# Optimization experiments

Measured on AMD Instinct MI355X. Metric: run time of the kernel, lower is better.

The kernel has to match this reference:

```python
import jax, jax.numpy as jnp
import numpy as np

B, T, N, NF, H, C, E = 4, 16, 4096, 8, 64, 13, 131072
NUM_HEADS = 4


def setup_inputs() -> dict:
    key = jax.random.key(0)
    ks = jax.random.split(key, 32)
    s = 0.05

    def w(k, shape):
        return (jax.random.normal(k, shape, jnp.float32) * s)

    p = {}
    p["node_features"] = jax.random.normal(ks[0], (B, T, N, NF), jnp.float32)
    p["edge_index_seq"] = jax.random.randint(ks[1], (T, 2, E), 0, N)
    # spatial_conv: Linear(NF,H) -> ReLU -> Linear(H,H)
    p["sc_w1"] = w(ks[2], (H, NF)); p["sc_b1"] = w(ks[3], (H,))
    p["sc_w2"] = w(ks[4], (H, H)); p["sc_b2"] = w(ks[5], (H,))
    # 2-layer LSTM (eval mode, dropout inactive); gate order i,f,g,o
    p["w_ih0"] = w(ks[6], (4 * H, H)); p["w_hh0"] = w(ks[7], (4 * H, H))
    p["b_ih0"] = w(ks[8], (4 * H,)); p["b_hh0"] = w(ks[9], (4 * H,))
    p["w_ih1"] = w(ks[10], (4 * H, H)); p["w_hh1"] = w(ks[11], (4 * H, H))
    p["b_ih1"] = w(ks[12], (4 * H,)); p["b_hh1"] = w(ks[13], (4 * H,))
    # MultiheadAttention (packed in-proj like torch)
    p["attn_in_w"] = w(ks[14], (3 * H, H)); p["attn_in_b"] = w(ks[15], (3 * H,))
    p["attn_out_w"] = w(ks[16], (H, H)); p["attn_out_b"] = w(ks[17], (H,))
    # predictor MLP (dropout inactive in eval)
    p["pw1"] = w(ks[18], (2 * H, H)); p["pb1"] = w(ks[19], (2 * H,))
    p["pw2"] = w(ks[20], (H, 2 * H)); p["pb2"] = w(ks[21], (H,))
    p["pw3"] = w(ks[22], (C, H)); p["pb3"] = w(ks[23], (C,))
    return p


def _message_pass(h_t, edges, n_nodes):
    # h_t: [B, N, H]; edges: [2, E]
    src, dst = edges[0], edges[1]
    msgs = h_t[:, src, :]  # gather pre-update embeddings, [B, E, H]
    sums = jax.vmap(lambda m: jax.ops.segment_sum(m, dst, num_segments=n_nodes))(msgs)
    cnt = jax.ops.segment_sum(jnp.ones(dst.shape, h_t.dtype), dst, num_segments=n_nodes)
    mean = sums / jnp.maximum(cnt, 1.0)[None, :, None]
    has_msg = (cnt > 0)[None, :, None]
    return jnp.where(has_msg, (h_t + mean) * 0.5, h_t)


def _lstm_layer(x, wi, wh, bi, bh):
    # x: [M, T, H] -> [M, T, H]
    M = x.shape[0]
    Hh = wh.shape[1]
    xg = x @ wi.T + bi  # precompute input contribution, [M, T, 4H]
    def step(carry, xg_t):
        hp, cp = carry
        g = xg_t + hp @ wh.T + bh
        i, f, gg, o = jnp.split(g, 4, axis=-1)
        i = jax.nn.sigmoid(i); f = jax.nn.sigmoid(f)
        gg = jnp.tanh(gg); o = jax.nn.sigmoid(o)
        c = f * cp + i * gg
        hn = o * jnp.tanh(c)
        return (hn, c), hn
    init = (jnp.zeros((M, Hh), x.dtype), jnp.zeros((M, Hh), x.dtype))
    _, hs = jax.lax.scan(step, init, xg.transpose(1, 0, 2))
    return hs.transpose(1, 0, 2)


def reference(node_features, edge_index_seq, sc_w1, sc_b1, sc_w2, sc_b2,
              w_ih0, w_hh0, b_ih0, b_hh0, w_ih1, w_hh1, b_ih1, b_hh1,
              attn_in_w, attn_in_b, attn_out_w, attn_out_b,
              pw1, pb1, pw2, pb2, pw3, pb3):
    Bs, Ts, Ns, _ = node_features.shape
    Hh = sc_w1.shape[0]

    # spatial conv over all timesteps at once: [B, T, N, H]
    h = jax.nn.relu(node_features @ sc_w1.T + sc_b1) @ sc_w2.T + sc_b2

    # per-timestep gather + segment-mean message passing (memory-bound core)
    def step(_, inp):
        h_t, e_t = inp
        return None, _message_pass(h_t, e_t, Ns)
    _, h_mp = jax.lax.scan(step, None, (h.transpose(1, 0, 2, 3), edge_index_seq))
    spatial_stack = h_mp.transpose(1, 0, 2, 3)  # [B, T, N, H]

    # LSTM over time per (batch, node)
    x = spatial_stack.transpose(0, 2, 1, 3).reshape(Bs * Ns, Ts, Hh)
    x = _lstm_layer(x, w_ih0, w_hh0, b_ih0, b_hh0)
    x = _lstm_layer(x, w_ih1, w_hh1, b_ih1, b_hh1)

    # self-attention (torch MHA, batch_first)
    qkv = x @ attn_in_w.T + attn_in_b
    q, k, v = jnp.split(qkv, 3, axis=-1)
    hd = Hh // NUM_HEADS
    def heads(z):
        return z.reshape(Bs * Ns, Ts, NUM_HEADS, hd).transpose(0, 2, 1, 3)
    q, k, v = heads(q), heads(k), heads(v)
    scores = jnp.einsum('mhqd,mhkd->mhqk', q, k) / np.float32(np.sqrt(hd))
    attn = jax.nn.softmax(scores, axis=-1)
    o = jnp.einsum('mhqk,mhkd->mhqd', attn, v)
    o = o.transpose(0, 2, 1, 3).reshape(Bs * Ns, Ts, Hh)
    o = o @ attn_out_w.T + attn_out_b

    final_hidden = o[:, -1, :]
    z = jax.nn.relu(final_hidden @ pw1.T + pb1)
    z = jax.nn.relu(z @ pw2.T + pb2)
    logits = z @ pw3.T + pb3
    return logits.reshape(Bs, Ns, -1)
```

## Files before the change

### kernel.cpp

```cpp
#include <hip/hip_runtime.h>

#define Bq 4
#define Tq 16
#define Nq 4096
#define NFq 8
#define Hq 64
#define Eq 131072
#define Cq 13
#define Mq (Bq*Nq)

typedef __attribute__((ext_vector_type(8))) short bf16x8;
typedef __attribute__((ext_vector_type(4))) float f32x4;

__device__ __forceinline__ float bf2f(unsigned short u) {
  return __uint_as_float(((unsigned int)u) << 16);
}
__device__ __forceinline__ unsigned short f2bf(float f) {
  unsigned int x = __float_as_uint(f);
  unsigned int r = x + 0x7fff + ((x >> 16) & 1);
  return (unsigned short)(r >> 16);
}
__device__ __forceinline__ float rcpf(float x) {
  float r;
  asm("v_rcp_f32 %0, %1" : "=v"(r) : "v"(x));
  return r;
}
__device__ __forceinline__ float sigf(float x) {
  return rcpf(1.f + __expf(-x));
}
__device__ __forceinline__ float tanh_c(float x) {
  float e = __expf(-2.f * x);
  return 2.f * rcpf(1.f + e) - 1.f;
}
__device__ __forceinline__ unsigned int pk_bf16(float lo, float hi) {
  unsigned int r;
  asm("v_cvt_pk_bf16_f32 %0, %1, %2" : "=v"(r) : "v"(lo), "v"(hi));
  return r;
}
__device__ __forceinline__ float dot2bf(unsigned int a, unsigned int b, float c) {
  float r;
  asm("v_dot2_f32_bf16 %0, %1, %2, %3" : "=v"(r) : "v"(a), "v"(b), "v"(c));
  return r;
}

#define O_BC0  65536
#define O_BC1  65792
#define O_QB   70144
#define O_VB   74304
#define O_B1P  95872

#define WB_AQT  0
#define WB_AWK  4096
#define WB_WVT  8192
#define WB_P1OW 12288
#define WB_P2T  20480
#define WB_P3T  28672
#define WB_TOT  29696

#define AQT_P   0
#define WVT_P   2048
#define P1OW_P  4096
#define P2T_P   8192
#define WAVE_SCR 3648
#define SMEM_ATTN (49152 + 8 * WAVE_SCR)

__global__ __launch_bounds__(256) void k_prep(
    const float* __restrict__ bih0, const float* __restrict__ bhh0,
    const float* __restrict__ bih1, const float* __restrict__ bhh1,
    float* __restrict__ wT) {
  int i = threadIdx.x;
  wT[O_BC0 + i] = bih0[i] + bhh0[i];
  wT[O_BC1 + i] = bih1[i] + bhh1[i];
}

__global__ __launch_bounds__(256) void k_prep_wa(
    const float* __restrict__ wih0, const float* __restrict__ whh0,
    const float* __restrict__ wih1, const float* __restrict__ whh1,
    unsigned short* __restrict__ WA) {
  int i = blockIdx.x * 256 + threadIdx.x;
  int j = i & 7, lane = (i >> 3) & 63, ks = (i >> 9) & 3;
  int mt = (i >> 11) & 15, L = (i >> 15) & 1;
  int rp = 16 * mt + (lane & 15);
  int orig = (rp & 3) * 64 + (rp >> 2);
  int k = 32 * ks + 8 * (lane >> 4) + j;
  const float* w = L ? (k < 64 ? wih1 : whh1) : (k < 64 ? wih0 : whh0);
  WA[i] = f2bf(w[orig * 64 + (k & 63)]);
}

__global__ __launch_bounds__(256) void k_prep2(
    const float* __restrict__ aw, const float* __restrict__ ab,
    const float* __restrict__ pw2, const float* __restrict__ pw3,
    unsigned short* __restrict__ WBu, float* __restrict__ wT) {
  int i = blockIdx.x * 256 + threadIdx.x;
  if (i < 4096) {
    int k = i >> 6, ch = i & 63;
    int pidx = (k >> 1) * 128 + ch * 2 + (k & 1);
    WBu[WB_AQT + pidx] = f2bf(0.25f * aw[ch * 64 + k]);
    WBu[WB_AWK + i]    = f2bf(aw[(64 + k) * 64 + ch]);
    WBu[WB_WVT + pidx] = f2bf(aw[(128 + ch) * 64 + k]);
  }
  {
    int k = i >> 6, j = i & 63;
    int pidx = (k >> 1) * 128 + j * 2 + (k & 1);
    WBu[WB_P2T + pidx] = f2bf(pw2[j * 128 + k]);
  }
  if (i < 1024) {
    int k = i >> 4, c = i & 15;
    int pidx = (k >> 1) * 32 + c * 2 + (k & 1);
    WBu[WB_P3T + pidx] = (c < 13) ? f2bf(pw3[c * 64 + k]) : (unsigned short)0;
  }
  if (i < 64) {
    wT[O_QB + i] = 0.25f * ab[i];
    wT[O_VB + i] = ab[128 + i];
  }
}

__global__ __launch_bounds__(256) void k_prep3(
    const float* __restrict__ pw1, const float* __restrict__ ow,
    const float* __restrict__ ob, const float* __restrict__ pb1,
    unsigned short* __restrict__ WBu, float* __restrict__ wT) {
  int i = blockIdx.x * 256 + threadIdx.x;
  int j = i >> 6, k = i & 63;
  float s0 = 0.f, s1 = 0.f, s2 = 0.f, s3 = 0.f;
  for (int m2 = 0; m2 < 64; m2 += 4) {
    s0 += pw1[j * 64 + m2]     * ow[m2 * 64 + k];
    s1 += pw1[j * 64 + m2 + 1] * ow[(m2 + 1) * 64 + k];
    s2 += pw1[j * 64 + m2 + 2] * ow[(m2 + 2) * 64 + k];
    s3 += pw1[j * 64 + m2 + 3] * ow[(m2 + 3) * 64 + k];
  }
  WBu[WB_P1OW + (k >> 1) * 256 + j * 2 + (k & 1)] = f2bf((s0 + s1) + (s2 + s3));
  if (k == 0) {
    float b = pb1[j];
    for (int m2 = 0; m2 < 64; ++m2) b += pw1[j * 64 + m2] * ob[m2];
    wT[O_B1P + j] = b;
  }
}

__global__ __launch_bounds__(256) void k_enc(
    const float* __restrict__ nf, const float* __restrict__ w1,
    const float* __restrict__ b1, const float* __restrict__ w2,
    const float* __restrict__ b2, unsigned short* __restrict__ henc) {
  __shared__ float xr[64][9];
  __shared__ float w1l[64][8];
  __shared__ float b1l[64];
  __shared__ float w2l[4096];
  __shared__ float b2l[64];
  __shared__ float h1l[64 * 65];
  __shared__ unsigned short OUT[64 * 68];
  int tid = threadIdx.x;
  size_t row0 = (size_t)blockIdx.x * 64;
  if (tid < 128) {
    float4 v = ((const float4*)w1)[tid];
    int j = tid >> 1, q = tid & 1;
    w1l[j][q * 4] = v.x; w1l[j][q * 4 + 1] = v.y;
    w1l[j][q * 4 + 2] = v.z; w1l[j][q * 4 + 3] = v.w;
  }
  if (tid < 64) { b1l[tid] = b1[tid]; b2l[tid] = b2[tid]; }
  {
    const float4* s = (const float4*)w2;
    #pragma unroll
    for (int u = 0; u < 4; ++u) {
      float4 v = s[tid + u * 256];
      int base = (tid + u * 256) * 4;
      w2l[base] = v.x; w2l[base + 1] = v.y; w2l[base + 2] = v.z; w2l[base + 3] = v.w;
    }
  }
  if (tid < 128) {
    float4 v = ((const float4*)(nf + row0 * 8))[tid];
    int r = tid >> 1, q = tid & 1;
    xr[r][q * 4] = v.x; xr[r][q * 4 + 1] = v.y;
    xr[r][q * 4 + 2] = v.z; xr[r][q * 4 + 3] = v.w;
  }
  __syncthreads();
  int r = tid & 63, co = tid >> 6;
  #pragma unroll
  for (int jj = 0; jj < 16; ++jj) {
    int j = co * 16 + jj;
    float acc = b1l[j];
    #pragma unroll
    for (int k = 0; k < 8; ++k) acc += w1l[j][k] * xr[r][k];
    h1l[r * 65 + j] = fmaxf(acc, 0.f);
  }
  __syncthreads();
  float acc[16];
  #pragma unroll
  for (int jj = 0; jj < 16; ++jj) acc[jj] = b2l[co * 16 + jj];
  for (int k = 0; k < 64; ++k) {
    float xv = h1l[r * 65 + k];
    #pragma unroll
    for (int jj = 0; jj < 16; ++jj)
      acc[jj] += w2l[(co * 16 + jj) * 64 + k] * xv;
  }
  #pragma unroll
  for (int jj = 0; jj < 16; jj += 2) {
    unsigned int pk = (unsigned int)f2bf(acc[jj]) | ((unsigned int)f2bf(acc[jj + 1]) << 16);
    *(unsigned int*)(&OUT[r * 68 + co * 16 + jj]) = pk;
  }
  __syncthreads();
  {
    int rr = tid >> 2, part = tid & 3;
    uint2 a = *(uint2*)(&OUT[rr * 68 + part * 16]);
    uint2 b = *(uint2*)(&OUT[rr * 68 + part * 16 + 4]);
    uint4 v; v.x = a.x; v.y = a.y; v.z = b.x; v.w = b.y;
    *(uint4*)(henc + (row0 + rr) * 64 + part * 16) = v;
  }
}

__global__ __launch_bounds__(1024) void k_count(const int* __restrict__ ei,
                                                int* __restrict__ bhist) {
  __shared__ int hist[4096];
  int b = blockIdx.x;
  int t = b & 15, seg = b >> 4;
  int tid = threadIdx.x;
  #pragma unroll
  for (int i = tid; i < 4096; i += 1024) hist[i] = 0;
  __syncthreads();
  const int* dstp = ei + ((t << 1) + 1) * Eq + (seg << 13);
  #pragma unroll
  for (int u = 0; u < 8; ++u) {
    int dst = dstp[(u << 10) + tid];
    atomicAdd(&hist[dst], 1);
  }
  __syncthreads();
  int* op = bhist + (b << 12);
  #pragma unroll
  for (int i = tid; i < 4096; i += 1024) op[i] = hist[i];
}

__global__ __launch_bounds__(256) void k_scan(const int* __restrict__ bhist,
                                              int* __restrict__ rp,
                                              int* __restrict__ segoff) {
  int t = blockIdx.x, tid = threadIdx.x;
  __shared__ int part[256];
  int loc[16];
  int s = 0;
  #pragma unroll
  for (int j = 0; j < 16; ++j) {
    int node = tid * 16 + j;
    int v = 0;
    #pragma unroll
    for (int seg = 0; seg < 16; ++seg)
      v += bhist[((t + (seg << 4)) << 12) + node];
    loc[j] = v;
    s += v;
  }
  part[tid] = s;
  __syncthreads();
  if (tid == 0) {
    int run = 0;
    for (int i2 = 0; i2 < 256; ++i2) { int v = part[i2]; part[i2] = run; run += v; }
  }
  __syncthreads();
  int off = part[tid];
  #pragma unroll
  for (int j = 0; j < 16; ++j) {
    int node = tid * 16 + j;
    rp[t * (Nq + 1) + node] = off;
    int running = off;
    #pragma unroll
    for (int seg = 0; seg < 16; ++seg) {
      segoff[(((t << 4) + seg) << 12) + node] = running;
      running += bhist[((t + (seg << 4)) << 12) + node];
    }
    off += loc[j];
  }
  if (tid == 255) rp[t * (Nq + 1) + Nq] = off;
}

__global__ __launch_bounds__(1024) void k_scatter(const int* __restrict__ ei,
    const int* __restrict__ segoff, int* __restrict__ col) {
  __shared__ int loff[4096];
  int b = blockIdx.x;
  int t = b & 15, seg = b >> 4;
  int tid = threadIdx.x;
  for (int i = tid; i < 4096; i += 1024)
    loff[i] = segoff[(((t << 4) + seg) << 12) + i];
  __syncthreads();
  const int* srcp = ei + (t << 1) * Eq + (seg << 13);
  const int* dstp = ei + ((t << 1) + 1) * Eq + (seg << 13);
  #pragma unroll
  for (int u = 0; u < 8; ++u) {
    int e = (u << 10) + tid;
    int src = srcp[e];
    int dst = dstp[e];
    int pos = atomicAdd(&loff[dst], 1);
    col[(t << 17) + pos] = src;
  }
}

__global__ __launch_bounds__(256) void k_mp(const unsigned short* __restrict__ henc,
    const int* __restrict__ rp, const int* __restrict__ col,
    unsigned short* __restrict__ hmp) {
  int lane = threadIdx.x & 63;
  int bkk = blockIdx.x;
  int t = bkk & 15;
  int n = (bkk >> 4) * 4 + __builtin_amdgcn_readfirstlane(threadIdx.x >> 6);
  const int* rpt = rp + t * (Nq + 1);
  const int* colt = col + (t << 17);
  int e0 = rpt[n], e1 = rpt[n + 1];
  int half = lane >> 5;
  int b2 = (lane >> 3) & 3;
  int c8 = (lane & 7) << 3;
  const unsigned short* hb2 = henc + (size_t)b2 * 4194304 + t * 262144 + c8;
  float acc[8] = {0.f, 0.f, 0.f, 0.f, 0.f, 0.f, 0.f, 0.f};
  int e = e0;
  for (; e + 8 <= e1; e += 8) {
    int i0 = colt[e + half];
    int i1 = colt[e + 2 + half];
    int i2 = colt[e + 4 + half];
    int i3 = colt[e + 6 + half];
    uint4 p0 = *(const uint4*)(hb2 + i0 * 64);
    uint4 p1 = *(const uint4*)(hb2 + i1 * 64);
    uint4 p2 = *(const uint4*)(hb2 + i2 * 64);
    uint4 p3 = *(const uint4*)(hb2 + i3 * 64);
    acc[0] += bf2f((unsigned short)(p0.x & 0xffff)) + bf2f((unsigned short)(p1.x & 0xffff))
            + bf2f((unsigned short)(p2.x & 0xffff)) + bf2f((unsigned short)(p3.x & 0xffff));
    acc[1] += bf2f((unsigned short)(p0.x >> 16)) + bf2f((unsigned short)(p1.x >> 16))
            + bf2f((unsigned short)(p2.x >> 16)) + bf2f((unsigned short)(p3.x >> 16));
    acc[2] += bf2f((unsigned short)(p0.y & 0xffff)) + bf2f((unsigned short)(p1.y & 0xffff))
            + bf2f((unsigned short)(p2.y & 0xffff)) + bf2f((unsigned short)(p3.y & 0xffff));
    acc[3] += bf2f((unsigned short)(p0.y >> 16)) + bf2f((unsigned short)(p1.y >> 16))
            + bf2f((unsigned short)(p2.y >> 16)) + bf2f((unsigned short)(p3.y >> 16));
    acc[4] += bf2f((unsigned short)(p0.z & 0xffff)) + bf2f((unsigned short)(p1.z & 0xffff))
            + bf2f((unsigned short)(p2.z & 0xffff)) + bf2f((unsigned short)(p3.z & 0xffff));
    acc[5] += bf2f((unsigned short)(p0.z >> 16)) + bf2f((unsigned short)(p1.z >> 16))
            + bf2f((unsigned short)(p2.z >> 16)) + bf2f((unsigned short)(p3.z >> 16));
    acc[6] += bf2f((unsigned short)(p0.w & 0xffff)) + bf2f((unsigned short)(p1.w & 0xffff))
            + bf2f((unsigned short)(p2.w & 0xffff)) + bf2f((unsigned short)(p3.w & 0xffff));
    acc[7] += bf2f((unsigned short)(p0.w >> 16)) + bf2f((unsigned short)(p1.w >> 16))
            + bf2f((unsigned short)(p2.w >> 16)) + bf2f((unsigned short)(p3.w >> 16));
  }
  if (half == 0) {
    for (; e < e1; ++e) {
      int i0 = colt[e];
      uint4 p0 = *(const uint4*)(hb2 + i0 * 64);
      acc[0] += bf2f((unsigned short)(p0.x & 0xffff));
      acc[1] += bf2f((unsigned short)(p0.x >> 16));
      acc[2] += bf2f((unsigned short)(p0.y & 0xffff));
      acc[3] += bf2f((unsigned short)(p0.y >> 16));
      acc[4] += bf2f((unsigned short)(p0.z & 0xffff));
      acc[5] += bf2f((unsigned short)(p0.z >> 16));
      acc[6] += bf2f((unsigned short)(p0.w & 0xffff));
      acc[7] += bf2f((unsigned short)(p0.w >> 16));
    }
  }
  #pragma unroll
  for (int i = 0; i < 8; ++i) acc[i] += __shfl_xor(acc[i], 32);
  uint4 ps = *(const uint4*)(hb2 + n * 64);
  int deg = e1 - e0;
  if (half == 0) {
    uint4 out;
    if (deg > 0) {
      float sc = 0.5f * rcpf((float)deg);
      float s0 = bf2f((unsigned short)(ps.x & 0xffff)) * 0.5f + acc[0] * sc;
      float s1 = bf2f((unsigned short)(ps.x >> 16))    * 0.5f + acc[1] * sc;
      float s2 = bf2f((unsigned short)(ps.y & 0xffff)) * 0.5f + acc[2] * sc;
      float s3 = bf2f((unsigned short)(ps.y >> 16))    * 0.5f + acc[3] * sc;
      float s4 = bf2f((unsigned short)(ps.z & 0xffff)) * 0.5f + acc[4] * sc;
      float s5 = bf2f((unsigned short)(ps.z >> 16))    * 0.5f + acc[5] * sc;
      float s6 = bf2f((unsigned short)(ps.w & 0xffff)) * 0.5f + acc[6] * sc;
      float s7 = bf2f((unsigned short)(ps.w >> 16))    * 0.5f + acc[7] * sc;
      out.x = pk_bf16(s0, s1);
      out.y = pk_bf16(s2, s3);
      out.z = pk_bf16(s4, s5);
      out.w = pk_bf16(s6, s7);
    } else {
      out = ps;
    }
    *(uint4*)(hmp + (size_t)b2 * 4194304 + t * 262144 + n * 64 + c8) = out;
  }
}

__global__ __launch_bounds__(1024) void k_lstm(
    const unsigned short* __restrict__ hmp,
    const unsigned short* __restrict__ WA,
    const float* __restrict__ wT,
    unsigned short* __restrict__ x2) {
  __shared__ unsigned short XF[4096];
  __shared__ unsigned short H0F[2][4096];
  __shared__ unsigned short H1F[2][4096];
  __shared__ unsigned short OUTB[64 * 68];
  int tid = threadIdx.x;
  int l = tid & 63;
  int w = tid >> 6;
  int mtp = w >> 1, ntp = w & 1;
  int m0 = blockIdx.x << 6;

  bf16x8 afr[2][2][4];
  const bf16x8* wa8 = (const bf16x8*)WA;
  #pragma unroll
  for (int L = 0; L < 2; ++L)
    #pragma unroll
    for (int mt2 = 0; mt2 < 2; ++mt2)
      #pragma unroll
      for (int ks = 0; ks < 4; ++ks)
        afr[L][mt2][ks] = wa8[((L * 16 + (2 * mtp + mt2)) * 4 + ks) * 64 + l];

  float4 bias0[2], bias1[2];
  int hbase[2], obase[2];
  #pragma unroll
  for (int mt2 = 0; mt2 < 2; ++mt2) {
    int ch = 4 * (2 * mtp + mt2) + (l >> 4);
    bias0[mt2].x = wT[O_BC0 + ch];       bias0[mt2].y = wT[O_BC0 + 64 + ch];
    bias0[mt2].z = wT[O_BC0 + 128 + ch]; bias0[mt2].w = wT[O_BC0 + 192 + ch];
    bias1[mt2].x = wT[O_BC1 + ch];       bias1[mt2].y = wT[O_BC1 + 64 + ch];
    bias1[mt2].z = wT[O_BC1 + 128 + ch]; bias1[mt2].w = wT[O_BC1 + 192 + ch];
    int l2 = (l & 15) | (((ch >> 3) & 3) << 4);
    hbase[mt2] = (ch >> 5) * 2048 + l2 * 8 + (ch & 7);
    obase[mt2] = (l & 15) * 68 + ch;
  }
  float c0a[2][2] = {{0.f, 0.f}, {0.f, 0.f}};
  float c1a[2][2] = {{0.f, 0.f}, {0.f, 0.f}};

  int sA = tid >> 4, c4 = (tid & 15) << 2;
  int xfidx = (((c4 >> 5) * 4 + (sA >> 4)) * 64 + ((sA & 15) | (((c4 >> 3) & 3) << 4))) * 8 + (c4 & 7);
  int mm = m0 + sA;
  int bb = mm >> 12, nn = mm & 4095;
  const unsigned short* srcb = hmp + ((size_t)(bb * 16) * 4096 + (size_t)nn) * 64 + c4;
  unsigned short* x2g = x2 + (size_t)mm * (Tq * Hq) + c4;
  int outsrc = sA * 68 + c4;

  int* hz0 = (int*)&H0F[0][0];
  int* hz1 = (int*)&H1F[0][0];
  for (int i = tid; i < 4096; i += 1024) { hz0[i] = 0; hz1[i] = 0; }

  uint2 xv = *(const uint2*)srcb;
  __syncthreads();

  for (int t = 0; t < Tq; ++t) {
    int cur = t & 1, prv = cur ^ 1;
    *(uint2*)(XF + xfidx) = xv;
    __syncthreads();
    if (t < Tq - 1) xv = *(const uint2*)(srcb + (t + 1) * 262144);

    {
      f32x4 acc[2][2];
      #pragma unroll
      for (int mt2 = 0; mt2 < 2; ++mt2)
        #pragma unroll
        for (int nt2 = 0; nt2 < 2; ++nt2) {
          float4 bv = bias0[mt2];
          acc[mt2][nt2] = (f32x4){bv.x, bv.y, bv.z, bv.w};
        }
      #pragma unroll
      for (int nt2 = 0; nt2 < 2; ++nt2) {
        int nt = 2 * ntp + nt2;
        #pragma unroll
        for (int ks = 0; ks < 4; ++ks) {
          const unsigned short* bs = (ks < 2) ? XF : H0F[prv];
          bf16x8 bf = *(const bf16x8*)(bs + (((ks & 1) * 4 + nt) * 64 + l) * 8);
          acc[0][nt2] = __builtin_amdgcn_mfma_f32_16x16x32_bf16(afr[0][0][ks], bf, acc[0][nt2], 0, 0, 0);
          acc[1][nt2] = __builtin_amdgcn_mfma_f32_16x16x32_bf16(afr[0][1][ks], bf, acc[1][nt2], 0, 0, 0);
        }
      }
      #pragma unroll
      for (int mt2 = 0; mt2 < 2; ++mt2) {
        float hh[2];
        #pragma unroll
        for (int nt2 = 0; nt2 < 2; ++nt2) {
          f32x4 g = acc[mt2][nt2];
          float ig = sigf(g[0]);
          float fg = sigf(g[1]);
          float gg = tanh_c(g[2]);
          float og = sigf(g[3]);
          float c = fg * c0a[mt2][nt2] + ig * gg;
          c0a[mt2][nt2] = c;
          hh[nt2] = og * tanh_c(c);
        }
        unsigned int pk = pk_bf16(hh[0], hh[1]);
        int base = hbase[mt2] + 2 * ntp * 512;
        H0F[cur][base]       = (unsigned short)pk;
        H0F[cur][base + 512] = (unsigned short)(pk >> 16);
      }
    }
    __syncthreads();

    {
      f32x4 acc[2][2];
      #pragma unroll
      for (int mt2 = 0; mt2 < 2; ++mt2)
        #pragma unroll
        for (int nt2 = 0; nt2 < 2; ++nt2) {
          float4 bv = bias1[mt2];
          acc[mt2][nt2] = (f32x4){bv.x, bv.y, bv.z, bv.w};
        }
      #pragma unroll
      for (int nt2 = 0; nt2 < 2; ++nt2) {
        int nt = 2 * ntp + nt2;
        #pragma unroll
        for (int ks = 0; ks < 4; ++ks) {
          const unsigned short* bs = (ks < 2) ? H0F[cur] : H1F[prv];
          bf16x8 bf = *(const bf16x8*)(bs + (((ks & 1) * 4 + nt) * 64 + l) * 8);
          acc[0][nt2] = __builtin_amdgcn_mfma_f32_16x16x32_bf16(afr[1][0][ks], bf, acc[0][nt2], 0, 0, 0);
          acc[1][nt2] = __builtin_amdgcn_mfma_f32_16x16x32_bf16(afr[1][1][ks], bf, acc[1][nt2], 0, 0, 0);
        }
      }
      #pragma unroll
      for (int mt2 = 0; mt2 < 2; ++mt2) {
        float hh[2];
        #pragma unroll
        for (int nt2 = 0; nt2 < 2; ++nt2) {
          f32x4 g = acc[mt2][nt2];
          float ig = sigf(g[0]);
          float fg = sigf(g[1]);
          float gg = tanh_c(g[2]);
          float og = sigf(g[3]);
          float c = fg * c1a[mt2][nt2] + ig * gg;
          c1a[mt2][nt2] = c;
          hh[nt2] = og * tanh_c(c);
        }
        unsigned int pk = pk_bf16(hh[0], hh[1]);
        int base = hbase[mt2] + 2 * ntp * 512;
        H1F[cur][base]       = (unsigned short)pk;
        H1F[cur][base + 512] = (unsigned short)(pk >> 16);
        int ob = obase[mt2] + 2 * ntp * 1088;
        OUTB[ob]        = (unsigned short)pk;
        OUTB[ob + 1088] = (unsigned short)(pk >> 16);
      }
    }
    __syncthreads();

    {
      uint2 ov = *(const uint2*)(OUTB + outsrc);
      *(uint2*)(x2g + t * 64) = ov;
    }
  }
}

__global__ __launch_bounds__(512, 4) void k_attn(const unsigned short* __restrict__ x2,
    const unsigned short* __restrict__ WB, const float* __restrict__ wp,
    const float* __restrict__ pb2, const float* __restrict__ pb3,
    float* __restrict__ outp) {
  extern __shared__ char smem[];
  unsigned int* WLu = (unsigned int*)smem;
  int tid = threadIdx.x;
  int lane = tid & 63;
  int wid = tid >> 6;
  {
    const uint4* src = (const uint4*)WB;
    uint4* dstw = (uint4*)smem;
    for (int i = tid; i < 3072; i += 512)
      dstw[i] = src[(i < 512) ? i : i + 512];
  }
  char* wbase = smem + 49152 + wid * WAVE_SCR;
  unsigned short* xw = (unsigned short*)wbase;
  float* q = (float*)(wbase + 2304);
  unsigned int* op = (unsigned int*)(wbase + 2304);
  unsigned int* qkp = (unsigned int*)(wbase + 2560);
  unsigned int* hbp = qkp;
  float* pz = (float*)(wbase + 3104);
  unsigned int* z2p = (unsigned int*)(wbase + 3104);
  unsigned int* z1p = (unsigned int*)(wbase + 3360);
  int m = (blockIdx.x << 3) + wid;
  {
    const uint4* xp = (const uint4*)(x2 + (size_t)m * 1024);
    #pragma unroll
    for (int u = 0; u < 2; ++u) {
      uint4 pv = xp[lane * 2 + u];
      int f0 = (lane * 2 + u) * 8;
      int t = f0 >> 6, ch0 = f0 & 63;
      *(uint4*)(xw + t * 72 + ch0) = pv;
    }
  }
  __syncthreads();
  {
    const unsigned short* xr = xw + 15 * 72;
    float a0 = wp[O_QB + lane], a1 = 0.f, a2 = 0.f, a3 = 0.f;
    #pragma unroll
    for (int k2 = 0; k2 < 32; k2 += 4) {
      a0 = dot2bf(WLu[AQT_P + (k2 + 0) * 64 + lane], *(const unsigned int*)(xr + 2 * (k2 + 0)), a0);
      a1 = dot2bf(WLu[AQT_P + (k2 + 1) * 64 + lane], *(const unsigned int*)(xr + 2 * (k2 + 1)), a1);
      a2 = dot2bf(WLu[AQT_P + (k2 + 2) * 64 + lane], *(const unsigned int*)(xr + 2 * (k2 + 2)), a2);
      a3 = dot2bf(WLu[AQT_P + (k2 + 3) * 64 + lane], *(const unsigned int*)(xr + 2 * (k2 + 3)), a3);
    }
    q[lane] = (a0 + a1) + (a2 + a3);
  }
  #pragma unroll
  for (int h = 0; h < 4; ++h) {
    float a0 = 0.f, a1 = 0.f, a2 = 0.f, a3 = 0.f;
    #pragma unroll
    for (int d = 0; d < 16; d += 4) {
      a0 += bf2f(WB[WB_AWK + (h * 16 + d + 0) * 64 + lane]) * q[h * 16 + d + 0];
      a1 += bf2f(WB[WB_AWK + (h * 16 + d + 1) * 64 + lane]) * q[h * 16 + d + 1];
      a2 += bf2f(WB[WB_AWK + (h * 16 + d + 2) * 64 + lane]) * q[h * 16 + d + 2];
      a3 += bf2f(WB[WB_AWK + (h * 16 + d + 3) * 64 + lane]) * q[h * 16 + d + 3];
    }
    float a = (a0 + a1) + (a2 + a3);
    float an = __shfl_xor(a, 1);
    if (!(lane & 1)) qkp[h * 33 + (lane >> 1)] = pk_bf16(a, an);
  }
  {
    int hh = lane >> 4, tt = lane & 15;
    const unsigned short* xr = xw + tt * 72;
    float a0 = 0.f, a1 = 0.f, a2 = 0.f, a3 = 0.f;
    #pragma unroll
    for (int c2 = 0; c2 < 32; c2 += 4) {
      a0 = dot2bf(qkp[hh * 33 + c2 + 0], *(const unsigned int*)(xr + 2 * (c2 + 0)), a0);
      a1 = dot2bf(qkp[hh * 33 + c2 + 1], *(const unsigned int*)(xr + 2 * (c2 + 1)), a1);
      a2 = dot2bf(qkp[hh * 33 + c2 + 2], *(const unsigned int*)(xr + 2 * (c2 + 2)), a2);
      a3 = dot2bf(qkp[hh * 33 + c2 + 3], *(const unsigned int*)(xr + 2 * (c2 + 3)), a3);
    }
    float sc = (a0 + a1) + (a2 + a3);
    float mx = sc;
    mx = fmaxf(mx, __shfl_xor(mx, 1));
    mx = fmaxf(mx, __shfl_xor(mx, 2));
    mx = fmaxf(mx, __shfl_xor(mx, 4));
    mx = fmaxf(mx, __shfl_xor(mx, 8));
    float e = __expf(sc - mx);
    float sum = e;
    sum += __shfl_xor(sum, 1);
    sum += __shfl_xor(sum, 2);
    sum += __shfl_xor(sum, 4);
    sum += __shfl_xor(sum, 8);
    pz[lane] = e * rcpf(sum);
  }
  {
    float hb0 = 0.f, hb1 = 0.f, hb2 = 0.f, hb3 = 0.f;
    #pragma unroll
    for (int t = 0; t < 16; ++t) {
      float xv = bf2f(xw[t * 72 + lane]);
      hb0 += pz[t] * xv;
      hb1 += pz[16 + t] * xv;
      hb2 += pz[32 + t] * xv;
      hb3 += pz[48 + t] * xv;
    }
    float n0 = __shfl_xor(hb0, 1);
    float n1 = __shfl_xor(hb1, 1);
    float n2 = __shfl_xor(hb2, 1);
    float n3 = __shfl_xor(hb3, 1);
    if (!(lane & 1)) {
      int p = lane >> 1;
      hbp[p]          = pk_bf16(hb0, n0);
      hbp[33 + p]     = pk_bf16(hb1, n1);
      hbp[66 + p]     = pk_bf16(hb2, n2);
      hbp[99 + p]     = pk_bf16(hb3, n3);
    }
  }
  {
    int hsel = lane >> 4;
    float a0 = wp[O_VB + lane], a1 = 0.f, a2 = 0.f, a3 = 0.f;
    #pragma unroll
    for (int k2 = 0; k2 < 32; k2 += 4) {
      a0 = dot2bf(WLu[WVT_P + (k2 + 0) * 64 + lane], hbp[hsel * 33 + k2 + 0], a0);
      a1 = dot2bf(WLu[WVT_P + (k2 + 1) * 64 + lane], hbp[hsel * 33 + k2 + 1], a1);
      a2 = dot2bf(WLu[WVT_P + (k2 + 2) * 64 + lane], hbp[hsel * 33 + k2 + 2], a2);
      a3 = dot2bf(WLu[WVT_P + (k2 + 3) * 64 + lane], hbp[hsel * 33 + k2 + 3], a3);
    }
    float o = (a0 + a1) + (a2 + a3);
    float on = __shfl_xor(o, 1);
    if (!(lane & 1)) op[lane >> 1] = pk_bf16(o, on);
  }
  {
    float a0 = wp[O_B1P + lane], a1 = 0.f;
    float b0 = wp[O_B1P + 64 + lane], b1 = 0.f;
    #pragma unroll
    for (int k2 = 0; k2 < 32; k2 += 2) {
      unsigned int ov0 = op[k2], ov1 = op[k2 + 1];
      a0 = dot2bf(WLu[P1OW_P + (k2 + 0) * 128 + lane], ov0, a0);
      a1 = dot2bf(WLu[P1OW_P + (k2 + 1) * 128 + lane], ov1, a1);
      b0 = dot2bf(WLu[P1OW_P + (k2 + 0) * 128 + 64 + lane], ov0, b0);
      b1 = dot2bf(WLu[P1OW_P + (k2 + 1) * 128 + 64 + lane], ov1, b1);
    }
    float ra = fmaxf(a0 + a1, 0.f);
    float rb = fmaxf(b0 + b1, 0.f);
    float ran = __shfl_xor(ra, 1);
    float rbn = __shfl_xor(rb, 1);
    if (!(lane & 1)) {
      z1p[lane >> 1]      = pk_bf16(ra, ran);
      z1p[32 + (lane >> 1)] = pk_bf16(rb, rbn);
    }
  }
  {
    float a0 = pb2[lane], a1 = 0.f, a2 = 0.f, a3 = 0.f;
    #pragma unroll
    for (int k2 = 0; k2 < 64; k2 += 4) {
      a0 = dot2bf(WLu[P2T_P + (k2 + 0) * 64 + lane], z1p[k2 + 0], a0);
      a1 = dot2bf(WLu[P2T_P + (k2 + 1) * 64 + lane], z1p[k2 + 1], a1);
      a2 = dot2bf(WLu[P2T_P + (k2 + 2) * 64 + lane], z1p[k2 + 2], a2);
      a3 = dot2bf(WLu[P2T_P + (k2 + 3) * 64 + lane], z1p[k2 + 3], a3);
    }
    float z2 = fmaxf((a0 + a1) + (a2 + a3), 0.f);
    float zn = __shfl_xor(z2, 1);
    if (!(lane & 1)) z2p[lane >> 1] = pk_bf16(z2, zn);
  }
  {
    const unsigned int* p3 = (const unsigned int*)(WB + WB_P3T);
    int c = lane & 15;
    float a0 = (c < 13) ? pb3[c] : 0.f, a1 = 0.f, a2 = 0.f, a3 = 0.f;
    #pragma unroll
    for (int k2 = 0; k2 < 32; k2 += 4) {
      a0 = dot2bf(p3[(k2 + 0) * 16 + c], z2p[k2 + 0], a0);
      a1 = dot2bf(p3[(k2 + 1) * 16 + c], z2p[k2 + 1], a1);
      a2 = dot2bf(p3[(k2 + 2) * 16 + c], z2p[k2 + 2], a2);
      a3 = dot2bf(p3[(k2 + 3) * 16 + c], z2p[k2 + 3], a3);
    }
    if (lane < 13) outp[(size_t)m * 13 + lane] = (a0 + a1) + (a2 + a3);
  }
}

extern "C" void kernel_launch(void* const* d_in, const int* in_sizes, int n_in,
                              void* d_out, int out_size, void* d_ws, size_t ws_size,
                              hipStream_t stream) {
  (void)in_sizes; (void)n_in; (void)out_size; (void)ws_size;
  const float* nf   = (const float*)d_in[0];
  const int*   ei   = (const int*)d_in[1];
  const float* sw1  = (const float*)d_in[2];
  const float* sb1  = (const float*)d_in[3];
  const float* sw2  = (const float*)d_in[4];
  const float* sb2  = (const float*)d_in[5];
  const float* wih0 = (const float*)d_in[6];
  const float* whh0 = (const float*)d_in[7];
  const float* bih0 = (const float*)d_in[8];
  const float* bhh0 = (const float*)d_in[9];
  const float* wih1 = (const float*)d_in[10];
  const float* whh1 = (const float*)d_in[11];
  const float* bih1 = (const float*)d_in[12];
  const float* bhh1 = (const float*)d_in[13];
  const float* aw   = (const float*)d_in[14];
  const float* ab   = (const float*)d_in[15];
  const float* ow   = (const float*)d_in[16];
  const float* ob   = (const float*)d_in[17];
  const float* pw1  = (const float*)d_in[18];
  const float* pb1  = (const float*)d_in[19];
  const float* pw2  = (const float*)d_in[20];
  const float* pb2  = (const float*)d_in[21];
  const float* pw3  = (const float*)d_in[22];
  const float* pb3  = (const float*)d_in[23];

  char* ws = (char*)d_ws;
  float* wT = (float*)ws;
  unsigned short* WA = (unsigned short*)(ws + 393216);
  unsigned short* WB = (unsigned short*)(ws + 458752);
  int* rp   = (int*)(ws + 1048576);
  int* col  = (int*)(ws + 1572864);
  unsigned short* henc = (unsigned short*)(ws + 10485760);
  unsigned short* hmp  = (unsigned short*)(ws + 44040192);
  int* bhist  = (int*)(ws + 44040192);
  int* segoff = (int*)(ws + 48234496);
  unsigned short* x2   = henc;
  float* outp = (float*)d_out;

  hipFuncSetAttribute((const void*)k_attn,
                      hipFuncAttributeMaxDynamicSharedMemorySize, SMEM_ATTN);
  k_prep<<<1, 256, 0, stream>>>(bih0, bhh0, bih1, bhh1, wT);
  k_prep_wa<<<256, 256, 0, stream>>>(wih0, whh0, wih1, whh1, WA);
  k_prep2<<<32, 256, 0, stream>>>(aw, ab, pw2, pw3, WB, wT);
  k_prep3<<<32, 256, 0, stream>>>(pw1, ow, ob, pb1, WB, wT);
  k_enc<<<4096, 256, 0, stream>>>(nf, sw1, sb1, sw2, sb2, henc);
  k_count<<<256, 1024, 0, stream>>>(ei, bhist);
  k_scan<<<16, 256, 0, stream>>>(bhist, rp, segoff);
  k_scatter<<<256, 1024, 0, stream>>>(ei, segoff, col);
  k_mp<<<16384, 256, 0, stream>>>(henc, rp, col, hmp);
  k_lstm<<<256, 1024, 0, stream>>>(hmp, WA, wT, x2);
  k_attn<<<2048, 512, SMEM_ATTN, stream>>>(x2, WB, wT, pb2, pb3, outp);
}
```

Before: 287.1 us.

## Halve LSTM block tile to 32 sequences so 512 blocks fill the GPU

The LSTM kernel now handles 32 sequences per 1024-thread block instead of 64. Each wave owns a single gate-channel m-tile across both n-tiles, and the launch grows to 512 blocks. The old 256-block grid underfills a GPU with 256 CUs and serialises the 16-step recurrence, so more blocks should give more latency hiding and better occupancy. In exchange, every block reloads the full weight fragments and shared-memory loads and stores become narrower, with more barriers per unit of work.

```diff
diff --git a/kernel.cpp b/kernel.cpp
--- a/kernel.cpp
+++ b/kernel.cpp
@@ -376,153 +376,123 @@
     const unsigned short* __restrict__ WA,
     const float* __restrict__ wT,
     unsigned short* __restrict__ x2) {
-  __shared__ unsigned short XF[4096];
-  __shared__ unsigned short H0F[2][4096];
-  __shared__ unsigned short H1F[2][4096];
-  __shared__ unsigned short OUTB[64 * 68];
+  __shared__ unsigned short XF[2048];
+  __shared__ unsigned short H0F[2][2048];
+  __shared__ unsigned short H1F[2][2048];
+  __shared__ unsigned short OUTB[32 * 68];
   int tid = threadIdx.x;
   int l = tid & 63;
-  int w = tid >> 6;
-  int mtp = w >> 1, ntp = w & 1;
-  int m0 = blockIdx.x << 6;
-
-  bf16x8 afr[2][2][4];
+  int w = __builtin_amdgcn_readfirstlane(tid >> 6);
+  int m0 = blockIdx.x << 5;
+
+  bf16x8 afr[2][4];
   const bf16x8* wa8 = (const bf16x8*)WA;
   #pragma unroll
   for (int L = 0; L < 2; ++L)
     #pragma unroll
-    for (int mt2 = 0; mt2 < 2; ++mt2)
-      #pragma unroll
-      for (int ks = 0; ks < 4; ++ks)
-        afr[L][mt2][ks] = wa8[((L * 16 + (2 * mtp + mt2)) * 4 + ks) * 64 + l];
-
-  float4 bias0[2], bias1[2];
-  int hbase[2], obase[2];
-  #pragma unroll
-  for (int mt2 = 0; mt2 < 2; ++mt2) {
-    int ch = 4 * (2 * mtp + mt2) + (l >> 4);
-    bias0[mt2].x = wT[O_BC0 + ch];       bias0[mt2].y = wT[O_BC0 + 64 + ch];
-    bias0[mt2].z = wT[O_BC0 + 128 + ch]; bias0[mt2].w = wT[O_BC0 + 192 + ch];
-    bias1[mt2].x = wT[O_BC1 + ch];       bias1[mt2].y = wT[O_BC1 + 64 + ch];
-    bias1[mt2].z = wT[O_BC1 + 128 + ch]; bias1[mt2].w = wT[O_BC1 + 192 + ch];
-    int l2 = (l & 15) | (((ch >> 3) & 3) << 4);
-    hbase[mt2] = (ch >> 5) * 2048 + l2 * 8 + (ch & 7);
-    obase[mt2] = (l & 15) * 68 + ch;
-  }
-  float c0a[2][2] = {{0.f, 0.f}, {0.f, 0.f}};
-  float c1a[2][2] = {{0.f, 0.f}, {0.f, 0.f}};
-
-  int sA = tid >> 4, c4 = (tid & 15) << 2;
-  int xfidx = (((c4 >> 5) * 4 + (sA >> 4)) * 64 + ((sA & 15) | (((c4 >> 3) & 3) << 4))) * 8 + (c4 & 7);
+    for (int ks = 0; ks < 4; ++ks)
+      afr[L][ks] = wa8[((L * 16 + w) * 4 + ks) * 64 + l];
+
+  int ch = 4 * w + (l >> 4);
+  float4 bias0, bias1;
+  bias0.x = wT[O_BC0 + ch];       bias0.y = wT[O_BC0 + 64 + ch];
+  bias0.z = wT[O_BC0 + 128 + ch]; bias0.w = wT[O_BC0 + 192 + ch];
+  bias1.x = wT[O_BC1 + ch];       bias1.y = wT[O_BC1 + 64 + ch];
+  bias1.z = wT[O_BC1 + 128 + ch]; bias1.w = wT[O_BC1 + 192 + ch];
+  int fl2 = (l & 15) | (((ch >> 3) & 3) << 4);
+  int hbase = (ch >> 5) * 1024 + fl2 * 8 + (ch & 7);
+  int obase = (l & 15) * 68 + ch;
+  float c0a[2] = {0.f, 0.f};
+  float c1a[2] = {0.f, 0.f};
+
+  int sA = tid >> 5, c2 = (tid & 31) << 1;
+  int xfidx = (((c2 >> 5) * 2 + (sA >> 4)) * 64 + ((sA & 15) | (((c2 >> 3) & 3) << 4))) * 8 + (c2 & 7);
   int mm = m0 + sA;
   int bb = mm >> 12, nn = mm & 4095;
-  const unsigned short* srcb = hmp + ((size_t)(bb * 16) * 4096 + (size_t)nn) * 64 + c4;
-  unsigned short* x2g = x2 + (size_t)mm * (Tq * Hq) + c4;
-  int outsrc = sA * 68 + c4;
+  const unsigned short* srcb = hmp + ((size_t)(bb * 16) * 4096 + (size_t)nn) * 64 + c2;
+  unsigned short* x2g = x2 + (size_t)mm * (Tq * Hq) + c2;
+  int outsrc = sA * 68 + c2;
 
   int* hz0 = (int*)&H0F[0][0];
   int* hz1 = (int*)&H1F[0][0];
-  for (int i = tid; i < 4096; i += 1024) { hz0[i] = 0; hz1[i] = 0; }
-
-  uint2 xv = *(const uint2*)srcb;
+  for (int i = tid; i < 2048; i += 1024) { hz0[i] = 0; hz1[i] = 0; }
+
+  unsigned int xv = *(const unsigned int*)srcb;
   __syncthreads();
 
   for (int t = 0; t < Tq; ++t) {
     int cur = t & 1, prv = cur ^ 1;
-    *(uint2*)(XF + xfidx) = xv;
+    *(unsigned int*)(XF + xfidx) = xv;
     __syncthreads();
-    if (t < Tq - 1) xv = *(const uint2*)(srcb + (t + 1) * 262144);
+    if (t < Tq - 1) xv = *(const unsigned int*)(srcb + (t + 1) * 262144);
 
     {
-      f32x4 acc[2][2];
+      f32x4 acc[2];
+      acc[0] = (f32x4){bias0.x, bias0.y, bias0.z, bias0.w};
+      acc[1] = acc[0];
       #pragma unroll
-      for (int mt2 = 0; mt2 < 2; ++mt2)
-        #pragma unroll
-        for (int nt2 = 0; nt2 < 2; ++nt2) {
-          float4 bv = bias0[mt2];
-          acc[mt2][nt2] = (f32x4){bv.x, bv.y, bv.z, bv.w};
-        }
-      #pragma unroll
-      for (int nt2 = 0; nt2 < 2; ++nt2) {
-        int nt = 2 * ntp + nt2;
+      for (int nt = 0; nt < 2; ++nt) {
         #pragma unroll
         for (int ks = 0; ks < 4; ++ks) {
           const unsigned short* bs = (ks < 2) ? XF : H0F[prv];
-          bf16x8 bf = *(const bf16x8*)(bs + (((ks & 1) * 4 + nt) * 64 + l) * 8);
-          acc[0][nt2] = __builtin_amdgcn_mfma_f32_16x16x32_bf16(afr[0][0][ks], bf, acc[0][nt2], 0, 0, 0);
-          acc[1][nt2] = __builtin_amdgcn_mfma_f32_16x16x32_bf16(afr[0][1][ks], bf, acc[1][nt2], 0, 0, 0);
+          bf16x8 bf = *(const bf16x8*)(bs + (((ks & 1) * 2 + nt) * 64 + l) * 8);
+          acc[nt] = __builtin_amdgcn_mfma_f32_16x16x32_bf16(afr[0][ks], bf, acc[nt], 0, 0, 0);
         }
       }
+      float hh[2];
       #pragma unroll
-      for (int mt2 = 0; mt2 < 2; ++mt2) {
-        float hh[2];
-        #pragma unroll
-        for (int nt2 = 0; nt2 < 2; ++nt2) {
-          f32x4 g = acc[mt2][nt2];
-          float ig = sigf(g[0]);
-          float fg = sigf(g[1]);
-          float gg = tanh_c(g[2]);
-          float og = sigf(g[3]);
-          float c = fg * c0a[mt2][nt2] + ig * gg;
-          c0a[mt2][nt2] = c;
-          hh[nt2] = og * tanh_c(c);
-        }
-        unsigned int pk = pk_bf16(hh[0], hh[1]);
-        int base = hbase[mt2] + 2 * ntp * 512;
-        H0F[cur][base]       = (unsigned short)pk;
-        H0F[cur][base + 512] = (unsigned short)(pk >> 16);
+      for (int nt = 0; nt < 2; ++nt) {
+        f32x4 g = acc[nt];
+        float ig = sigf(g[0]);
+        float fg = sigf(g[1]);
+        float gg = tanh_c(g[2]);
+        float og = sigf(g[3]);
+        float c = fg * c0a[nt] + ig * gg;
+        c0a[nt] = c;
+        hh[nt] = og * tanh_c(c);
       }
+      unsigned int pk = pk_bf16(hh[0], hh[1]);
+      H0F[cur][hbase]       = (unsigned short)pk;
+      H0F[cur][hbase + 512] = (unsigned short)(pk >> 16);
     }
     __syncthreads();
 
     {
-      f32x4 acc[2][2];
+      f32x4 acc[2];
+      acc[0] = (f32x4){bias1.x, bias1.y, bias1.z, bias1.w};
+      acc[1] = acc[0];
       #pragma unroll
-      for (int mt2 = 0; mt2 < 2; ++mt2)
-        #pragma unroll
-        for (int nt2 = 0; nt2 < 2; ++nt2) {
-          float4 bv = bias1[mt2];
-          acc[mt2][nt2] = (f32x4){bv.x, bv.y, bv.z, bv.w};
-        }
-      #pragma unroll
-      for (int nt2 = 0; nt2 < 2; ++nt2) {
-        int nt = 2 * ntp + nt2;
+      for (int nt = 0; nt < 2; ++nt) {
         #pragma unroll
         for (int ks = 0; ks < 4; ++ks) {
           const unsigned short* bs = (ks < 2) ? H0F[cur] : H1F[prv];
-          bf16x8 bf = *(const bf16x8*)(bs + (((ks & 1) * 4 + nt) * 64 + l) * 8);
-          acc[0][nt2] = __builtin_amdgcn_mfma_f32_16x16x32_bf16(afr[1][0][ks], bf, acc[0][nt2], 0, 0, 0);
-          acc[1][nt2] = __builtin_amdgcn_mfma_f32_16x16x32_bf16(afr[1][1][ks], bf, acc[1][nt2], 0, 0, 0);
+          bf16x8 bf = *(const bf16x8*)(bs + (((ks & 1) * 2 + nt) * 64 + l) * 8);
+          acc[nt] = __builtin_amdgcn_mfma_f32_16x16x32_bf16(afr[1][ks], bf, acc[nt], 0, 0, 0);
         }
       }
+      float hh[2];
       #pragma unroll
-      for (int mt2 = 0; mt2 < 2; ++mt2) {
-        float hh[2];
-        #pragma unroll
-        for (int nt2 = 0; nt2 < 2; ++nt2) {
-          f32x4 g = acc[mt2][nt2];
-          float ig = sigf(g[0]);
-          float fg = sigf(g[1]);
-          float gg = tanh_c(g[2]);
-          float og = sigf(g[3]);
-          float c = fg * c1a[mt2][nt2] + ig * gg;
-          c1a[mt2][nt2] = c;
-          hh[nt2] = og * tanh_c(c);
-        }
-        unsigned int pk = pk_bf16(hh[0], hh[1]);
-        int base = hbase[mt2] + 2 * ntp * 512;
-        H1F[cur][base]       = (unsigned short)pk;
-        H1F[cur][base + 512] = (unsigned short)(pk >> 16);
-        int ob = obase[mt2] + 2 * ntp * 1088;
-        OUTB[ob]        = (unsigned short)pk;
-        OUTB[ob + 1088] = (unsigned short)(pk >> 16);
+      for (int nt = 0; nt < 2; ++nt) {
+        f32x4 g = acc[nt];
+        float ig = sigf(g[0]);
+        float fg = sigf(g[1]);
+        float gg = tanh_c(g[2]);
+        float og = sigf(g[3]);
+        float c = fg * c1a[nt] + ig * gg;
+        c1a[nt] = c;
+        hh[nt] = og * tanh_c(c);
       }
+      unsigned int pk = pk_bf16(hh[0], hh[1]);
+      H1F[cur][hbase]       = (unsigned short)pk;
+      H1F[cur][hbase + 512] = (unsigned short)(pk >> 16);
+      OUTB[obase]        = (unsigned short)pk;
+      OUTB[obase + 1088] = (unsigned short)(pk >> 16);
     }
     __syncthreads();
 
     {
-      uint2 ov = *(const uint2*)(OUTB + outsrc);
-      *(uint2*)(x2g + t * 64) = ov;
+      unsigned int ov = *(const unsigned int*)(OUTB + outsrc);
+      *(unsigned int*)(x2g + t * 64) = ov;
     }
   }
 }
@@ -751,6 +721,6 @@
   k_scan<<<16, 256, 0, stream>>>(bhist, rp, segoff);
   k_scatter<<<256, 1024, 0, stream>>>(ei, segoff, col);
   k_mp<<<16384, 256, 0, stream>>>(henc, rp, col, hmp);
-  k_lstm<<<256, 1024, 0, stream>>>(hmp, WA, wT, x2);
+  k_lstm<<<512, 1024, 0, stream>>>(hmp, WA, wT, x2);
   k_attn<<<2048, 512, SMEM_ATTN, stream>>>(x2, WB, wT, pb2, pb3, outp);
 }
```

Measured after the change: 289.6 us. About the same (+0.9%).
